# Optimization experiments

Measured on AMD Instinct MI355X. Metric: run time of the kernel, lower is better.

The kernel has to match this reference:

```python
import jax, jax.numpy as jnp
import numpy as np

# dims per init_kwargs / input_specs
B, S, HID = 4, 2048, 1024
H = 16          # num_heads
DH = HID // H   # head_dim = 64
G = 1024        # group_size; grouped feature dim = S*DH//G = 128
SCALE = 1.0 / (DH ** 0.5)


def setup_inputs() -> dict:
    key = jax.random.key(0)
    ks = jax.random.split(key, 9)
    w = lambda k: jax.random.normal(k, (HID, HID), jnp.float32) * 0.02
    b = lambda k: jax.random.normal(k, (HID,), jnp.float32) * 0.02
    return {
        "hidden_states": jax.random.normal(ks[0], (B, S, HID), jnp.float32),
        "Wq": w(ks[1]), "bq": b(ks[2]),
        "Wk": w(ks[3]), "bk": b(ks[4]),
        "Wv": w(ks[5]), "bv": b(ks[6]),
        "Wo": w(ks[7]), "bo": b(ks[8]),
    }


def reference(hidden_states, Wq, bq, Wk, bk, Wv, bv, Wo, bo):
    Bs, Ss, _ = hidden_states.shape

    def proj(W, bias):
        # torch nn.Linear: x @ W.T + b
        y = hidden_states @ W.T + bias                      # [B,S,HID]
        y = y.reshape(Bs, Ss, H, DH).transpose(0, 2, 1, 3)  # [B,H,S,DH]
        # grouped view: fold seq/head_dim into G groups of S*DH//G features
        return y.reshape(Bs, H, G, -1)                      # [B,H,G,S*DH/G]

    q, k, v = proj(Wq, bq), proj(Wk, bk), proj(Wv, bv)
    scores = jnp.einsum("bhgd,bhkd->bhgk", q, k) * SCALE    # [B,H,G,G]
    probs = jax.nn.softmax(scores, axis=-1)                 # dropout: eval mode (identity)
    ctx = jnp.einsum("bhgk,bhkd->bhgd", probs, v)           # [B,H,G,S*DH/G]
    ctx = ctx.transpose(0, 2, 1, 3).reshape(Bs, -1, HID)    # [B,S,HID]
    return ctx @ Wo.T + bo
```

## Files before the change

kernel.cpp:

```cpp
#include <hip/hip_runtime.h>


typedef __attribute__((ext_vector_type(8))) short short8;
typedef __attribute__((ext_vector_type(4))) float f32x4;
typedef unsigned int u32;
typedef unsigned short u16;

#define MFMA16(a, b, c) __builtin_amdgcn_mfma_f32_16x16x32_bf16((a), (b), (c), 0, 0, 0)

union S8 { short8 s; uint2 v[2]; u32 u[4]; };

__device__ __forceinline__ u32 f2bf1(float x) {
    union { float f; u32 u; } v; v.f = x;
    return (v.u + 0x7fffu + ((v.u >> 16) & 1u)) >> 16;
}

__device__ __forceinline__ void gld16(u16* lds, const u16* g) {
    __builtin_amdgcn_global_load_lds(
        (const __attribute__((address_space(1))) unsigned int*)(g),
        (__attribute__((address_space(3))) unsigned int*)(lds),
        16, 0, 0);
}

__global__ __launch_bounds__(256) void convert(
    const float* __restrict__ X, const float* __restrict__ Wq,
    const float* __restrict__ Wk, const float* __restrict__ Wv,
    const float* __restrict__ Wo,
    u16* __restrict__ Xb, u16* __restrict__ Wcat, u16* __restrict__ Wob)
{
    const size_t M8 = 8388608, M1 = 1048576;
    size_t i = ((size_t)blockIdx.x * 256 + threadIdx.x) * 16;
    const float* src; u16* dst;
    if (i < M8)              { src = X  + i;                dst = Xb   + i; }
    else if (i < M8 + M1)    { src = Wq + (i - M8);         dst = Wcat + (i - M8); }
    else if (i < M8 + 2*M1)  { src = Wk + (i - M8 - M1);    dst = Wcat + (i - M8); }
    else if (i < M8 + 3*M1)  { src = Wv + (i - M8 - 2*M1);  dst = Wcat + (i - M8); }
    else                     { src = Wo + (i - M8 - 3*M1);  dst = Wob  + (i - M8 - 3*M1); }
#pragma unroll
    for (int j = 0; j < 2; ++j) {
        float4 a = ((const float4*)src)[2 * j];
        float4 b = ((const float4*)src)[2 * j + 1];
        uint4 o;
        o.x = f2bf1(a.x) | (f2bf1(a.y) << 16);
        o.y = f2bf1(a.z) | (f2bf1(a.w) << 16);
        o.z = f2bf1(b.x) | (f2bf1(b.y) << 16);
        o.w = f2bf1(b.z) | (f2bf1(b.w) << 16);
        ((uint4*)dst)[j] = o;
    }
}

__global__ __launch_bounds__(256, 3) void qkv_gemm9(
    const u16* __restrict__ Xb, const u16* __restrict__ Wcat,
    const float* __restrict__ b0, const float* __restrict__ b1,
    const float* __restrict__ b2,
    u16* __restrict__ q_att, u16* __restrict__ k_att, u16* __restrict__ v_t)
{
    const int nb = blockIdx.x, mb = blockIdx.y;
    const int mat = nb >> 3;

    __shared__ __align__(16) u16 As[128 * 64];
    __shared__ __align__(16) u16 Bs[128 * 64];

    const int t = threadIdx.x, wave = t >> 6, lane = t & 63;
    const int l15 = lane & 15, quad = lane >> 4;
    const int wm = (wave >> 1) * 64, wn = (wave & 1) * 64;

    const int srow = t >> 3;
    const int scol = ((t & 7) ^ (srow & 7)) * 8;
    u16* ldsA = As + wave * 512;
    u16* ldsB = Bs + wave * 512;

    const u16* Ab = Xb   + (size_t)(mb * 128) * 1024;
    const u16* Bb = Wcat + (size_t)(nb * 128) * 1024;

    const int swz = l15 & 7;

    f32x4 acc[4][4] = {};

    for (int k0 = 0; k0 < 1024; k0 += 64) {
        __syncthreads();
#pragma unroll
        for (int c = 0; c < 4; ++c) {
            size_t so = (size_t)(c * 32 + srow) * 1024 + k0 + scol;
            gld16(ldsA + c * 2048, Ab + so);
            gld16(ldsB + c * 2048, Bb + so);
        }
        __syncthreads();

#pragma unroll
        for (int ks = 0; ks < 2; ++ks) {
            short8 af[4], bf[4];
            const int ck = ((ks * 4 + quad) ^ swz) * 8;
#pragma unroll
            for (int mt = 0; mt < 4; ++mt)
                af[mt] = *(const short8*)(As + (wm + mt * 16 + l15) * 64 + ck);
#pragma unroll
            for (int nt = 0; nt < 4; ++nt)
                bf[nt] = *(const short8*)(Bs + (wn + nt * 16 + l15) * 64 + ck);
#pragma unroll
            for (int mt = 0; mt < 4; ++mt)
#pragma unroll
                for (int nt = 0; nt < 4; ++nt)
                    acc[mt][nt] = MFMA16(af[mt], bf[nt], acc[mt][nt]);
        }
    }

    const float* bias = (mat == 0) ? b0 : (mat == 1) ? b1 : b2;
    const float scl = (mat == 0) ? 0.125f : 1.0f;
#pragma unroll
    for (int nt = 0; nt < 4; ++nt) {
        int colm = (nb & 7) * 128 + wn + nt * 16 + l15;
        float bv = bias[colm];
        int h = colm >> 6, dh = colm & 63;
#pragma unroll
        for (int mt = 0; mt < 4; ++mt) {
            int row0 = mb * 128 + wm + mt * 16 + quad * 4;
            int b = row0 >> 11, s0 = row0 & 2047;
            int bh = b * 16 + h, g0 = s0 >> 1;
            float v0 = (acc[mt][nt][0] + bv) * scl, v1 = (acc[mt][nt][1] + bv) * scl;
            float v2 = (acc[mt][nt][2] + bv) * scl, v3 = (acc[mt][nt][3] + bv) * scl;
            if (mat == 2) {
                u32 w0 = f2bf1(v0) | (f2bf1(v2) << 16);
                u32 w1 = f2bf1(v1) | (f2bf1(v3) << 16);
                int j6 = g0 & 63;
                int gp = (g0 & ~63) + (j6 & 32) + ((j6 >> 2) & 3) * 8
                       + ((j6 >> 4) & 1) * 4 + (j6 & 3);
                *(u32*)(v_t + ((size_t)(bh * 128 + dh) * 1024 + gp)) = w0;
                *(u32*)(v_t + ((size_t)(bh * 128 + dh + 64) * 1024 + gp)) = w1;
            } else {
                u16* dst = (mat == 0) ? q_att : k_att;
                u32 w0 = f2bf1(v0) | (f2bf1(v1) << 16);
                u32 w1 = f2bf1(v2) | (f2bf1(v3) << 16);
                size_t base = ((size_t)bh * 1024 + g0) * 128 + 2 * dh;
                *(u32*)(dst + base) = w0;
                *(u32*)(dst + base + 128) = w1;
            }
        }
    }
}

__global__ __launch_bounds__(256) void attn4(
    const u16* __restrict__ q_att, const u16* __restrict__ k_att,
    const u16* __restrict__ v_t, u16* __restrict__ ctx)
{
    const int bh = blockIdx.y, qb = blockIdx.x;
    const u16* Q = q_att + (size_t)bh * 131072;
    const u16* K = k_att + (size_t)bh * 131072;
    const u16* V = v_t  + (size_t)bh * 131072;

    __shared__ __align__(16) u16 Ks[64 * 128];
    __shared__ __align__(16) u16 Vs[128 * 64];

    const int t = threadIdx.x, wave = t >> 6, lane = t & 63;
    const int l15 = lane & 15, quad = lane >> 4;
    const int q_row = qb * 64 + wave * 16 + l15;

    int offK[4], offV[4];
#pragma unroll
    for (int j = 0; j < 4; ++j) {
        int ck = wave * 4 + j;
        int rowK = ck * 4 + (lane >> 4);
        offK[j] = rowK * 128 + (((lane & 15) ^ (rowK & 15)) * 8);
        int rowV = ck * 8 + (lane >> 3);
        offV[j] = rowV * 1024 + (((lane & 7) ^ ((lane >> 3) & 7)) * 8);
    }

    short8 bq[4];
#pragma unroll
    for (int kb = 0; kb < 4; ++kb)
        bq[kb] = *(const short8*)(Q + (size_t)q_row * 128 + kb * 32 + quad * 8);

    f32x4 accO[8] = {};
    float m_i = -1e30f, l_i = 0.0f;

    for (int kt = 0; kt < 16; ++kt) {
        const u16* Kt = K + (size_t)kt * 8192;
        const u16* Vt = V + (size_t)kt * 64;
        __syncthreads();
#pragma unroll
        for (int j = 0; j < 4; ++j) {
            gld16(Ks + (wave * 4 + j) * 512, Kt + offK[j]);
            gld16(Vs + (wave * 4 + j) * 512, Vt + offV[j]);
        }
        __syncthreads();

        f32x4 accS[4] = {};
#pragma unroll
        for (int kf = 0; kf < 4; ++kf)
#pragma unroll
            for (int kb = 0; kb < 4; ++kb) {
                short8 ak = *(const short8*)(Ks + (kf * 16 + l15) * 128
                                             + (((kb * 4 + quad) ^ l15) * 8));
                accS[kf] = MFMA16(ak, bq[kb], accS[kf]);
            }

        float mloc = -1e30f;
#pragma unroll
        for (int kf = 0; kf < 4; ++kf)
            mloc = fmaxf(mloc, fmaxf(fmaxf(accS[kf][0], accS[kf][1]),
                                     fmaxf(accS[kf][2], accS[kf][3])));
        mloc = fmaxf(mloc, __shfl_xor(mloc, 16));
        mloc = fmaxf(mloc, __shfl_xor(mloc, 32));
        float mn = fmaxf(m_i, mloc);
        float alpha = __expf(m_i - mn);
        m_i = mn;

        float lsum = 0.0f;
        u32 pb[8];
#pragma unroll
        for (int kf = 0; kf < 4; ++kf) {
            float p0 = __expf(accS[kf][0] - mn);
            float p1 = __expf(accS[kf][1] - mn);
            float p2 = __expf(accS[kf][2] - mn);
            float p3 = __expf(accS[kf][3] - mn);
            lsum += (p0 + p1) + (p2 + p3);
            pb[kf * 2]     = f2bf1(p0) | (f2bf1(p1) << 16);
            pb[kf * 2 + 1] = f2bf1(p2) | (f2bf1(p3) << 16);
        }
        lsum += __shfl_xor(lsum, 16);
        lsum += __shfl_xor(lsum, 32);
        l_i = l_i * alpha + lsum;

#pragma unroll
        for (int f = 0; f < 8; ++f) {
            accO[f][0] *= alpha; accO[f][1] *= alpha;
            accO[f][2] *= alpha; accO[f][3] *= alpha;
        }

        S8 bp0, bp1;
        bp0.u[0] = pb[0]; bp0.u[1] = pb[1]; bp0.u[2] = pb[2]; bp0.u[3] = pb[3];
        bp1.u[0] = pb[4]; bp1.u[1] = pb[5]; bp1.u[2] = pb[6]; bp1.u[3] = pb[7];
        const int l7 = l15 & 7;
#pragma unroll
        for (int df = 0; df < 8; ++df) {
            const u16* vrow = Vs + (df * 16 + l15) * 64;
            short8 av0 = *(const short8*)(vrow + ((quad ^ l7) * 8));
            short8 av1 = *(const short8*)(vrow + (((quad + 4) ^ l7) * 8));
            accO[df] = MFMA16(av0, bp0.s, accO[df]);
            accO[df] = MFMA16(av1, bp1.s, accO[df]);
        }
    }

    const int h = bh & 15, b = bh >> 4;
    float inv = 1.0f / l_i;
    size_t base = ((size_t)(b * 2048 + 2 * q_row + (h >> 3))) * 1024 + (h & 7) * 128;
#pragma unroll
    for (int df = 0; df < 8; ++df) {
        int dp = df * 16 + quad * 4;
        uint2 w;
        w.x = f2bf1(accO[df][0] * inv) | (f2bf1(accO[df][1] * inv) << 16);
        w.y = f2bf1(accO[df][2] * inv) | (f2bf1(accO[df][3] * inv) << 16);
        *(uint2*)(ctx + base + dp) = w;
    }
}

__global__ __launch_bounds__(256, 3) void out_gemm9(
    const u16* __restrict__ ctx, const u16* __restrict__ Wob,
    const float* __restrict__ bo, float* __restrict__ out)
{
    const int nb = blockIdx.x, mb = blockIdx.y;
    __shared__ __align__(16) u16 As[128 * 64];
    __shared__ __align__(16) u16 Bs[128 * 64];
    const int t = threadIdx.x, wave = t >> 6, lane = t & 63;
    const int l15 = lane & 15, quad = lane >> 4;
    const int wm = (wave >> 1) * 64, wn = (wave & 1) * 64;

    const int srow = t >> 3;
    const int scol = ((t & 7) ^ (srow & 7)) * 8;
    u16* ldsA = As + wave * 512;
    u16* ldsB = Bs + wave * 512;

    const u16* Ab = ctx + (size_t)(mb * 128) * 1024;
    const u16* Bb = Wob + (size_t)(nb * 128) * 1024;

    const int swz = l15 & 7;

    f32x4 acc[4][4] = {};

    for (int k0 = 0; k0 < 1024; k0 += 64) {
        __syncthreads();
#pragma unroll
        for (int c = 0; c < 4; ++c) {
            size_t so = (size_t)(c * 32 + srow) * 1024 + k0 + scol;
            gld16(ldsA + c * 2048, Ab + so);
            gld16(ldsB + c * 2048, Bb + so);
        }
        __syncthreads();

#pragma unroll
        for (int ks = 0; ks < 2; ++ks) {
            short8 af[4], bf[4];
            const int ck = ((ks * 4 + quad) ^ swz) * 8;
#pragma unroll
            for (int mt = 0; mt < 4; ++mt)
                af[mt] = *(const short8*)(As + (wm + mt * 16 + l15) * 64 + ck);
#pragma unroll
            for (int nt = 0; nt < 4; ++nt)
                bf[nt] = *(const short8*)(Bs + (wn + nt * 16 + l15) * 64 + ck);
#pragma unroll
            for (int mt = 0; mt < 4; ++mt)
#pragma unroll
                for (int nt = 0; nt < 4; ++nt)
                    acc[mt][nt] = MFMA16(af[mt], bf[nt], acc[mt][nt]);
        }
    }

#pragma unroll
    for (int nt = 0; nt < 4; ++nt) {
        int col = nb * 128 + wn + nt * 16 + l15;
        float bv = bo[col];
#pragma unroll
        for (int mt = 0; mt < 4; ++mt)
#pragma unroll
            for (int r = 0; r < 4; ++r) {
                int row = mb * 128 + wm + mt * 16 + quad * 4 + r;
                out[(size_t)row * 1024 + col] = acc[mt][nt][r] + bv;
            }
    }
}

extern "C" void kernel_launch(void* const* d_in, const int* in_sizes, int n_in,
                              void* d_out, int out_size, void* d_ws, size_t ws_size,
                              hipStream_t stream)
{
    const float* X  = (const float*)d_in[0];
    const float* Wq = (const float*)d_in[1];
    const float* bq = (const float*)d_in[2];
    const float* Wk = (const float*)d_in[3];
    const float* bk = (const float*)d_in[4];
    const float* Wv = (const float*)d_in[5];
    const float* bv = (const float*)d_in[6];
    const float* Wo = (const float*)d_in[7];
    const float* bo = (const float*)d_in[8];

    const size_t M8 = 8388608;
    u16* q_att = (u16*)d_ws;
    u16* k_att = q_att + M8;
    u16* v_t   = k_att + M8;
    u16* Xb    = v_t   + M8;
    u16* ctx   = Xb;
    u16* Wcat  = Xb + M8;
    u16* Wob   = Wcat + 3 * 1048576;

    convert<<<dim3(3072), 256, 0, stream>>>(X, Wq, Wk, Wv, Wo, Xb, Wcat, Wob);
    qkv_gemm9<<<dim3(24, 64), 256, 0, stream>>>(Xb, Wcat, bq, bk, bv,
                                                q_att, k_att, v_t);
    attn4<<<dim3(16, 64), 256, 0, stream>>>(q_att, k_att, v_t, ctx);
    out_gemm9<<<dim3(8, 64), 256, 0, stream>>>(ctx, Wob, bo, (float*)d_out);
}
```

Measured before the change: 263.7 us.

## Double-buffer attention K/V tiles and process two query groups per wave

Rewrites the attention kernel so each wave handles 32 query rows (two 16-row groups) that share the K/V fragments. The next K/V tile is loaded into a second LDS buffer while the current one is computed, leaving one barrier per iteration. It also adds a lazy softmax rescale that only runs when the running max rises by more than 8, hardware packed bf16 conversion for the probabilities, MFMA priority hints, and a swapped grid order so blocks of the same head run together. The costs are more registers per thread and twice the LDS, which can lower occupancy, and a wider exponent range in the unnormalised accumulators.

```diff
diff --git a/kernel.cpp b/kernel.cpp
--- a/kernel.cpp
+++ b/kernel.cpp
@@ -13,6 +13,12 @@
 __device__ __forceinline__ u32 f2bf1(float x) {
     union { float f; u32 u; } v; v.f = x;
     return (v.u + 0x7fffu + ((v.u >> 16) & 1u)) >> 16;
+}
+
+__device__ __forceinline__ u32 cvtpk(float lo, float hi) {
+    u32 r;
+    asm("v_cvt_pk_bf16_f32 %0, %1, %2" : "=v"(r) : "v"(lo), "v"(hi));
+    return r;
 }
 
 __device__ __forceinline__ void gld16(u16* lds, const u16* g) {
@@ -139,21 +145,20 @@
     }
 }
 
-__global__ __launch_bounds__(256) void attn4(
+__global__ __launch_bounds__(256, 2) void attn5(
     const u16* __restrict__ q_att, const u16* __restrict__ k_att,
     const u16* __restrict__ v_t, u16* __restrict__ ctx)
 {
-    const int bh = blockIdx.y, qb = blockIdx.x;
+    const int bh = blockIdx.x, qb = blockIdx.y;
     const u16* Q = q_att + (size_t)bh * 131072;
     const u16* K = k_att + (size_t)bh * 131072;
     const u16* V = v_t  + (size_t)bh * 131072;
 
-    __shared__ __align__(16) u16 Ks[64 * 128];
-    __shared__ __align__(16) u16 Vs[128 * 64];
+    __shared__ __align__(16) u16 Ks[2][64 * 128];
+    __shared__ __align__(16) u16 Vs[2][128 * 64];
 
     const int t = threadIdx.x, wave = t >> 6, lane = t & 63;
     const int l15 = lane & 15, quad = lane >> 4;
-    const int q_row = qb * 64 + wave * 16 + l15;
 
     int offK[4], offV[4];
 #pragma unroll
@@ -165,92 +170,127 @@
         offV[j] = rowV * 1024 + (((lane & 7) ^ ((lane >> 3) & 7)) * 8);
     }
 
-    short8 bq[4];
-#pragma unroll
-    for (int kb = 0; kb < 4; ++kb)
-        bq[kb] = *(const short8*)(Q + (size_t)q_row * 128 + kb * 32 + quad * 8);
-
-    f32x4 accO[8] = {};
-    float m_i = -1e30f, l_i = 0.0f;
+#define ASTAGE(pp, kt) do {                                                   \
+        const u16* Kt_ = K + (size_t)(kt) * 8192;                             \
+        const u16* Vt_ = V + (size_t)(kt) * 64;                               \
+        _Pragma("unroll")                                                     \
+        for (int j_ = 0; j_ < 4; ++j_) {                                      \
+            gld16(&Ks[(pp)][(wave * 4 + j_) * 512], Kt_ + offK[j_]);          \
+            gld16(&Vs[(pp)][(wave * 4 + j_) * 512], Vt_ + offV[j_]);          \
+        }                                                                     \
+    } while (0)
+
+    short8 bq[2][4];
+#pragma unroll
+    for (int qg = 0; qg < 2; ++qg) {
+        const int qr = qb * 128 + wave * 32 + qg * 16 + l15;
+#pragma unroll
+        for (int kb = 0; kb < 4; ++kb)
+            bq[qg][kb] = *(const short8*)(Q + (size_t)qr * 128 + kb * 32 + quad * 8);
+    }
+
+    f32x4 accO[2][8] = {};
+    float m_i[2] = {-1e30f, -1e30f}, l_i[2] = {0.0f, 0.0f};
+
+    ASTAGE(0, 0);
+    __syncthreads();
 
     for (int kt = 0; kt < 16; ++kt) {
-        const u16* Kt = K + (size_t)kt * 8192;
-        const u16* Vt = V + (size_t)kt * 64;
-        __syncthreads();
-#pragma unroll
-        for (int j = 0; j < 4; ++j) {
-            gld16(Ks + (wave * 4 + j) * 512, Kt + offK[j]);
-            gld16(Vs + (wave * 4 + j) * 512, Vt + offV[j]);
-        }
-        __syncthreads();
-
-        f32x4 accS[4] = {};
+        const int p = kt & 1;
+        if (kt + 1 < 16) ASTAGE(p ^ 1, kt + 1);
+        const u16* Ksp = &Ks[p][0];
+        const u16* Vsp = &Vs[p][0];
+
+        f32x4 accS[2][4] = {};
+        __builtin_amdgcn_s_setprio(1);
 #pragma unroll
         for (int kf = 0; kf < 4; ++kf)
 #pragma unroll
             for (int kb = 0; kb < 4; ++kb) {
-                short8 ak = *(const short8*)(Ks + (kf * 16 + l15) * 128
+                short8 ak = *(const short8*)(Ksp + (kf * 16 + l15) * 128
                                              + (((kb * 4 + quad) ^ l15) * 8));
-                accS[kf] = MFMA16(ak, bq[kb], accS[kf]);
-            }
-
-        float mloc = -1e30f;
-#pragma unroll
-        for (int kf = 0; kf < 4; ++kf)
-            mloc = fmaxf(mloc, fmaxf(fmaxf(accS[kf][0], accS[kf][1]),
-                                     fmaxf(accS[kf][2], accS[kf][3])));
-        mloc = fmaxf(mloc, __shfl_xor(mloc, 16));
-        mloc = fmaxf(mloc, __shfl_xor(mloc, 32));
-        float mn = fmaxf(m_i, mloc);
-        float alpha = __expf(m_i - mn);
-        m_i = mn;
-
-        float lsum = 0.0f;
-        u32 pb[8];
-#pragma unroll
-        for (int kf = 0; kf < 4; ++kf) {
-            float p0 = __expf(accS[kf][0] - mn);
-            float p1 = __expf(accS[kf][1] - mn);
-            float p2 = __expf(accS[kf][2] - mn);
-            float p3 = __expf(accS[kf][3] - mn);
-            lsum += (p0 + p1) + (p2 + p3);
-            pb[kf * 2]     = f2bf1(p0) | (f2bf1(p1) << 16);
-            pb[kf * 2 + 1] = f2bf1(p2) | (f2bf1(p3) << 16);
-        }
-        lsum += __shfl_xor(lsum, 16);
-        lsum += __shfl_xor(lsum, 32);
-        l_i = l_i * alpha + lsum;
-
-#pragma unroll
-        for (int f = 0; f < 8; ++f) {
-            accO[f][0] *= alpha; accO[f][1] *= alpha;
-            accO[f][2] *= alpha; accO[f][3] *= alpha;
-        }
-
-        S8 bp0, bp1;
-        bp0.u[0] = pb[0]; bp0.u[1] = pb[1]; bp0.u[2] = pb[2]; bp0.u[3] = pb[3];
-        bp1.u[0] = pb[4]; bp1.u[1] = pb[5]; bp1.u[2] = pb[6]; bp1.u[3] = pb[7];
+                accS[0][kf] = MFMA16(ak, bq[0][kb], accS[0][kf]);
+                accS[1][kf] = MFMA16(ak, bq[1][kb], accS[1][kf]);
+            }
+        __builtin_amdgcn_s_setprio(0);
+
+        u32 pb[2][8];
+#pragma unroll
+        for (int qg = 0; qg < 2; ++qg) {
+            float mloc = -1e30f;
+#pragma unroll
+            for (int kf = 0; kf < 4; ++kf)
+                mloc = fmaxf(mloc, fmaxf(fmaxf(accS[qg][kf][0], accS[qg][kf][1]),
+                                         fmaxf(accS[qg][kf][2], accS[qg][kf][3])));
+            mloc = fmaxf(mloc, __shfl_xor(mloc, 16));
+            mloc = fmaxf(mloc, __shfl_xor(mloc, 32));
+
+            if (!__all(mloc - m_i[qg] <= 8.0f)) {
+                float mn = fmaxf(m_i[qg], mloc);
+                float alpha = __expf(m_i[qg] - mn);
+#pragma unroll
+                for (int f = 0; f < 8; ++f) {
+                    accO[qg][f][0] *= alpha; accO[qg][f][1] *= alpha;
+                    accO[qg][f][2] *= alpha; accO[qg][f][3] *= alpha;
+                }
+                l_i[qg] *= alpha;
+                m_i[qg] = mn;
+            }
+
+            float lsum = 0.0f;
+            const float mi = m_i[qg];
+#pragma unroll
+            for (int kf = 0; kf < 4; ++kf) {
+                float p0 = __expf(accS[qg][kf][0] - mi);
+                float p1 = __expf(accS[qg][kf][1] - mi);
+                float p2 = __expf(accS[qg][kf][2] - mi);
+                float p3 = __expf(accS[qg][kf][3] - mi);
+                lsum += (p0 + p1) + (p2 + p3);
+                pb[qg][kf * 2]     = cvtpk(p0, p1);
+                pb[qg][kf * 2 + 1] = cvtpk(p2, p3);
+            }
+            lsum += __shfl_xor(lsum, 16);
+            lsum += __shfl_xor(lsum, 32);
+            l_i[qg] += lsum;
+        }
+
+        S8 bp00, bp01, bp10, bp11;
+        bp00.u[0] = pb[0][0]; bp00.u[1] = pb[0][1]; bp00.u[2] = pb[0][2]; bp00.u[3] = pb[0][3];
+        bp01.u[0] = pb[0][4]; bp01.u[1] = pb[0][5]; bp01.u[2] = pb[0][6]; bp01.u[3] = pb[0][7];
+        bp10.u[0] = pb[1][0]; bp10.u[1] = pb[1][1]; bp10.u[2] = pb[1][2]; bp10.u[3] = pb[1][3];
+        bp11.u[0] = pb[1][4]; bp11.u[1] = pb[1][5]; bp11.u[2] = pb[1][6]; bp11.u[3] = pb[1][7];
         const int l7 = l15 & 7;
+        __builtin_amdgcn_s_setprio(1);
 #pragma unroll
         for (int df = 0; df < 8; ++df) {
-            const u16* vrow = Vs + (df * 16 + l15) * 64;
+            const u16* vrow = Vsp + (df * 16 + l15) * 64;
             short8 av0 = *(const short8*)(vrow + ((quad ^ l7) * 8));
             short8 av1 = *(const short8*)(vrow + (((quad + 4) ^ l7) * 8));
-            accO[df] = MFMA16(av0, bp0.s, accO[df]);
-            accO[df] = MFMA16(av1, bp1.s, accO[df]);
-        }
-    }
+            accO[0][df] = MFMA16(av0, bp00.s, accO[0][df]);
+            accO[0][df] = MFMA16(av1, bp01.s, accO[0][df]);
+            accO[1][df] = MFMA16(av0, bp10.s, accO[1][df]);
+            accO[1][df] = MFMA16(av1, bp11.s, accO[1][df]);
+        }
+        __builtin_amdgcn_s_setprio(0);
+
+        if (kt + 1 < 16) __syncthreads();
+    }
+#undef ASTAGE
 
     const int h = bh & 15, b = bh >> 4;
-    float inv = 1.0f / l_i;
-    size_t base = ((size_t)(b * 2048 + 2 * q_row + (h >> 3))) * 1024 + (h & 7) * 128;
-#pragma unroll
-    for (int df = 0; df < 8; ++df) {
-        int dp = df * 16 + quad * 4;
-        uint2 w;
-        w.x = f2bf1(accO[df][0] * inv) | (f2bf1(accO[df][1] * inv) << 16);
-        w.y = f2bf1(accO[df][2] * inv) | (f2bf1(accO[df][3] * inv) << 16);
-        *(uint2*)(ctx + base + dp) = w;
+#pragma unroll
+    for (int qg = 0; qg < 2; ++qg) {
+        const int qr = qb * 128 + wave * 32 + qg * 16 + l15;
+        float inv = 1.0f / l_i[qg];
+        size_t base = ((size_t)(b * 2048 + 2 * qr + (h >> 3))) * 1024 + (h & 7) * 128;
+#pragma unroll
+        for (int df = 0; df < 8; ++df) {
+            int dp = df * 16 + quad * 4;
+            uint2 w;
+            w.x = f2bf1(accO[qg][df][0] * inv) | (f2bf1(accO[qg][df][1] * inv) << 16);
+            w.y = f2bf1(accO[qg][df][2] * inv) | (f2bf1(accO[qg][df][3] * inv) << 16);
+            *(uint2*)(ctx + base + dp) = w;
+        }
     }
 }
 
@@ -345,6 +385,6 @@
     convert<<<dim3(3072), 256, 0, stream>>>(X, Wq, Wk, Wv, Wo, Xb, Wcat, Wob);
     qkv_gemm9<<<dim3(24, 64), 256, 0, stream>>>(Xb, Wcat, bq, bk, bv,
                                                 q_att, k_att, v_t);
-    attn4<<<dim3(16, 64), 256, 0, stream>>>(q_att, k_att, v_t, ctx);
+    attn5<<<dim3(64, 8), 256, 0, stream>>>(q_att, k_att, v_t, ctx);
     out_gemm9<<<dim3(8, 64), 256, 0, stream>>>(ctx, Wob, bo, (float*)d_out);
 }
```

Result: faster. 238.1 us (-9.7%).
